# Performance work log

Measured on AMD Instinct MI355X. Metric: run time of the kernel, lower is better.

## Reference

```python
import jax, jax.numpy as jnp
import numpy as np

N = 50000      # nodes
E = 800000     # edges per relation (avg degree 16)
D = 128        # in_feat == out_feat
H = 4          # num_heads
DH = D // H    # head dim = 32
NEG_SLOPE = 0.2  # DGL GATConv default


def setup_inputs() -> dict:
    key = jax.random.key(0)
    ks = jax.random.split(key, 12)
    inp = {
        "x": jax.random.normal(ks[0], (N, D), jnp.float32),
        "W_r0": jax.random.normal(ks[1], (D, D), jnp.float32) * (1.0 / np.sqrt(D)),
        "attn_l_r0": jax.random.normal(ks[2], (H, DH), jnp.float32),
        "attn_r_r0": jax.random.normal(ks[3], (H, DH), jnp.float32),
        "W_r1": jax.random.normal(ks[4], (D, D), jnp.float32) * (1.0 / np.sqrt(D)),
        "attn_l_r1": jax.random.normal(ks[5], (H, DH), jnp.float32),
        "attn_r_r1": jax.random.normal(ks[6], (H, DH), jnp.float32),
        "loop_weight": jax.random.normal(ks[7], (D, D), jnp.float32) * (1.0 / np.sqrt(D)),
        "h_bias": jnp.zeros((D,), jnp.float32),
        "src_r0": jax.random.randint(ks[8], (E,), 0, N, jnp.int32),
        "dst_r0": jax.random.randint(ks[9], (E,), 0, N, jnp.int32),
        "src_r1": jax.random.randint(ks[10], (E,), 0, N, jnp.int32),
        "dst_r1": jax.random.randint(ks[11], (E,), 0, N, jnp.int32),
    }
    return inp


def _gat_conv(x, W, attn_l, attn_r, src, dst):
    """One DGL-style GATConv (no bias, no conv activation). Returns [N,H,DH]."""
    feat = (x @ W).reshape(N, H, DH)                 # projected features
    el = jnp.einsum('nhd,hd->nh', feat, attn_l)      # [N,H] attn on source
    er = jnp.einsum('nhd,hd->nh', feat, attn_r)      # [N,H] attn on dest
    e = jax.nn.leaky_relu(el[src] + er[dst], NEG_SLOPE)  # [E,H]
    # edge softmax over incoming edges of each dst node (stable)
    emax = jax.ops.segment_max(e, dst, num_segments=N)   # [N,H]
    ex = jnp.exp(e - emax[dst])                          # [E,H]
    denom = jax.ops.segment_sum(ex, dst, num_segments=N) # [N,H]
    alpha = ex / denom[dst]                              # [E,H]
    msg = feat[src] * alpha[:, :, None]                  # [E,H,DH]
    return jax.ops.segment_sum(msg, dst, num_segments=N) # [N,H,DH]


def reference(x, W_r0, attn_l_r0, attn_r_r0, W_r1, attn_l_r1, attn_r_r1,
              loop_weight, h_bias, src_r0, dst_r0, src_r1, dst_r1):
    # HeteroGraphConv with default 'sum' cross-relation aggregation
    h = _gat_conv(x, W_r0, attn_l_r0, attn_r_r0, src_r0, dst_r0) \
      + _gat_conv(x, W_r1, attn_l_r1, attn_r_r1, src_r1, dst_r1)
    h = h.reshape(N, H * DH)          # flatten heads -> [N, out_feat]
    h = h + x @ loop_weight           # self loop
    h = h + h_bias                    # bias
    h = jax.nn.relu(h)                # activation (dropout=0, no norm, no FFN)
    return h
```

## Files before the change

kernel.cpp:

```cpp
#include <hip/hip_runtime.h>
#include <hip/hip_bf16.h>

#define NN 50000
#define EE 800000
#define DD 128
#define HH 4
#define NEG_SLOPE 0.2f

#define BSH 9
#define NBUCK 98
#define CH 8192
#define NBLK 98
#define NSEG (2 * NBUCK * NBLK)
#define BKB (2 * NBLK)
#define SORTB (2 * NBUCK)
#define ELRB 3125
#define PJB ((NN + 127) / 128)
#define WB 192

typedef __attribute__((ext_vector_type(8))) short bf16x8;
typedef __attribute__((ext_vector_type(4))) float f32x4;
typedef __attribute__((ext_vector_type(8))) unsigned short ushrt8;

static __device__ __forceinline__ float bf2f(ushort u) {
    union { unsigned int ui; float f; } v; v.ui = ((unsigned int)u) << 16; return v.f;
}
static __device__ __forceinline__ void split1(float v, ushort& h, ushort& l) {
    __hip_bfloat16 hb = __float2bfloat16(v);
    float hf = __bfloat162float(hb);
    __hip_bfloat16 lb = __float2bfloat16(v - hf);
    h = *(ushort*)&hb; l = *(ushort*)&lb;
}

__global__ __launch_bounds__(256) void prep_kernel(
    const float* __restrict__ W0, const float* __restrict__ W1,
    const float* __restrict__ Wl,
    const float* __restrict__ al0, const float* __restrict__ ar0,
    const float* __restrict__ al1, const float* __restrict__ ar1,
    const int* __restrict__ dst0, const int* __restrict__ dst1,
    ushort* __restrict__ wt, float* __restrict__ uvec, int* __restrict__ hist)
{
    const int b = blockIdx.x;
    const int t = threadIdx.x;
    if (b < WB) {
        int idx = b * 256 + t;
        int m = idx >> 14, e = idx & 16383;
        const float* W = (m == 0) ? W0 : (m == 1) ? W1 : Wl;
        int k = e >> 7, n = e & 127;
        ushort h, l; split1(W[e], h, l);
        int q = m * 4 + (k >> 5);
        int kin8 = (k >> 3) & 3, ke = k & 7;
        int sw = n & 7;
        size_t base = (size_t)q * 8192 + n * 64;
        wt[base + (((0 | kin8) ^ sw) << 3) + ke] = h;
        wt[base + (((4 | kin8) ^ sw) << 3) + ke] = l;
    } else if (b < WB + BKB) {
        __shared__ int cnt[NBUCK];
        int hb = b - WB;
        int rel = hb >= NBLK;
        int ci = hb - rel * NBLK;
        const int* __restrict__ dstA = rel ? dst1 : dst0;
        if (t < NBUCK) cnt[t] = 0;
        __syncthreads();
        int lo = ci * CH, hi = min(lo + CH, EE);
        for (int i = lo + t; i < hi; i += 256)
            atomicAdd(&cnt[dstA[i] >> BSH], 1);
        __syncthreads();
        if (t < NBUCK)
            hist[((rel * NBUCK) + t) * NBLK + ci] = cnt[t];
    } else {
        #pragma unroll
        for (int j = 0; j < 8; ++j) {
            int idx = t * 8 + j;
            int v = idx >> 7, k = idx & 127;
            int rel = v >> 3, lr = (v >> 2) & 1, h = v & 3;
            const float* W = rel ? W1 : W0;
            const float* a = rel ? (lr ? ar1 : al1) : (lr ? ar0 : al0);
            float s = 0.f;
            for (int d2 = 0; d2 < 32; ++d2)
                s += W[k * 128 + h * 32 + d2] * a[h * 32 + d2];
            uvec[v * 128 + k] = s;
        }
    }
}

__global__ __launch_bounds__(256) void scan_kernel(
    const int* __restrict__ hist, int* __restrict__ base)
{
    __shared__ int wq[4];
    const int t = threadIdx.x;
    const int lane = t & 63, wv = t >> 6;
    const int st = t * 76;
    const int en = min(st + 76, NSEG);
    int sum = 0;
    for (int i = st; i < en; ++i) sum += hist[i];
    int incl = sum;
    #pragma unroll
    for (int off = 1; off < 64; off <<= 1) {
        int u = __shfl_up(incl, off);
        if (lane >= off) incl += u;
    }
    if (lane == 63) wq[wv] = incl;
    __syncthreads();
    int woff = 0;
    #pragma unroll
    for (int w = 0; w < 4; ++w) woff += (w < wv) ? wq[w] : 0;
    int run = woff + incl - sum;
    for (int i = st; i < en; ++i) { base[i] = run; run += hist[i]; }
}

__global__ __launch_bounds__(256) void bucketelr_kernel(
    const int* __restrict__ src0, const int* __restrict__ dst0,
    const int* __restrict__ src1, const int* __restrict__ dst1,
    const int* __restrict__ base, unsigned int* __restrict__ pk,
    const float* __restrict__ x, const float* __restrict__ uvec,
    float* __restrict__ el0, float* __restrict__ er0,
    float* __restrict__ el1, float* __restrict__ er1)
{
    __shared__ float sm[2048];
    const int t = threadIdx.x;

    if (blockIdx.x < BKB) {
        int* cnt = (int*)sm;
        int* bs  = cnt + 128;
        const int hb = blockIdx.x;
        const int rel = hb >= NBLK;
        const int ci = hb - rel * NBLK;
        const int* __restrict__ srcA = rel ? src1 : src0;
        const int* __restrict__ dstA = rel ? dst1 : dst0;
        if (t < NBUCK) {
            cnt[t] = 0;
            bs[t] = base[((rel * NBUCK) + t) * NBLK + ci];
        }
        __syncthreads();
        int lo = ci * CH, hi = min(lo + CH, EE);
        for (int i = lo + t; i < hi; i += 256) {
            int dd = dstA[i], ss = srcA[i];
            int bk = dd >> BSH;
            int rk = atomicAdd(&cnt[bk], 1);
            pk[bs[bk] + rk] = (unsigned int)ss | ((unsigned int)(dd & 511) << 17);
        }
        return;
    }

    for (int i = t; i < 2048; i += 256) sm[i] = uvec[i];
    __syncthreads();
    const int lane = t & 63, wave = t >> 6;
    const int l16 = lane & 15;
    const int r = (blockIdx.x - BKB) * 16 + wave * 4 + (lane >> 4);
    float xr[8];
    if (r < NN) {
        float4 a = *(const float4*)&x[(size_t)r * DD + l16 * 8];
        float4 b2 = *(const float4*)&x[(size_t)r * DD + l16 * 8 + 4];
        xr[0] = a.x; xr[1] = a.y; xr[2] = a.z; xr[3] = a.w;
        xr[4] = b2.x; xr[5] = b2.y; xr[6] = b2.z; xr[7] = b2.w;
    } else {
        #pragma unroll
        for (int j = 0; j < 8; ++j) xr[j] = 0.f;
    }
    float s[16];
    #pragma unroll
    for (int v = 0; v < 16; ++v) {
        float acc = 0.f;
        const float* u = &sm[v * 128 + l16 * 8];
        #pragma unroll
        for (int j = 0; j < 8; ++j) acc += xr[j] * u[j];
        s[v] = acc;
    }
    #pragma unroll
    for (int m = 1; m < 16; m <<= 1)
        #pragma unroll
        for (int v = 0; v < 16; ++v) s[v] += __shfl_xor(s[v], m);
    if (r < NN) {
        float val = s[0];
        #pragma unroll
        for (int v = 1; v < 16; ++v) val = (l16 == v) ? s[v] : val;
        float* p = (l16 & 8) ? ((l16 & 4) ? er1 : el1)
                             : ((l16 & 4) ? er0 : el0);
        p[(size_t)r * 4 + (l16 & 3)] = val;
    }
}

__global__ __launch_bounds__(256) void proj_kernel(
    const float* __restrict__ x, const ushort* __restrict__ wt,
    const float* __restrict__ bias,
    ushort* __restrict__ fb0, ushort* __restrict__ fb1,
    float* __restrict__ out)
{
    __shared__ ushort lds[2][8192];
    const int t = threadIdx.x;
    const int lane = t & 63, wave = t >> 6;
    const int l15 = lane & 15, lg = lane >> 4;
    const int rb = blockIdx.x * 128 + wave * 32;

    int ra0 = rb + l15;      if (ra0 > NN - 1) ra0 = NN - 1;
    int ra1 = rb + 16 + l15; if (ra1 > NN - 1) ra1 = NN - 1;
    const int kb = lg * 8;

    bf16x8 Ah0[4], Av0[4], Ah1[4], Av1[4];
    #pragma unroll
    for (int kc = 0; kc < 4; ++kc) {
        const float* p0 = &x[(size_t)ra0 * DD + kc * 32 + kb];
        const float* p1 = &x[(size_t)ra1 * DD + kc * 32 + kb];
        float4 f0a = *(const float4*)p0, f0b = *(const float4*)(p0 + 4);
        float4 f1a = *(const float4*)p1, f1b = *(const float4*)(p1 + 4);
        float t0[8] = {f0a.x, f0a.y, f0a.z, f0a.w, f0b.x, f0b.y, f0b.z, f0b.w};
        float t1[8] = {f1a.x, f1a.y, f1a.z, f1a.w, f1b.x, f1b.y, f1b.z, f1b.w};
        union { bf16x8 v; ushort u[8]; } H0, L0, H1, L1;
        #pragma unroll
        for (int j = 0; j < 8; ++j) {
            split1(t0[j], H0.u[j], L0.u[j]);
            split1(t1[j], H1.u[j], L1.u[j]);
        }
        Ah0[kc] = H0.v; Av0[kc] = L0.v;
        Ah1[kc] = H1.v; Av1[kc] = L1.v;
    }

    {
        const bf16x8* g = (const bf16x8*)wt;
        bf16x8* L = (bf16x8*)lds[0];
        #pragma unroll
        for (int i = 0; i < 4; ++i) L[t + i * 256] = g[t + i * 256];
    }

    for (int m = 0; m < 3; ++m) {
        f32x4 acc0[8], acc1[8];
        #pragma unroll
        for (int nt = 0; nt < 8; ++nt) {
            acc0[nt] = (f32x4){0.f, 0.f, 0.f, 0.f};
            acc1[nt] = (f32x4){0.f, 0.f, 0.f, 0.f};
        }

        #pragma unroll
        for (int kc = 0; kc < 4; ++kc) {
            const int q = m * 4 + kc;
            __syncthreads();
            bf16x8 st0, st1, st2, st3;
            const bool hasNext = (q < 11);
            if (hasNext) {
                const bf16x8* g = (const bf16x8*)(wt + (size_t)(q + 1) * 8192);
                st0 = g[t]; st1 = g[t + 256]; st2 = g[t + 512]; st3 = g[t + 768];
            }
            const ushort* __restrict__ L = lds[kc & 1];
            #pragma unroll
            for (int nt = 0; nt < 8; ++nt) {
                const int n = nt * 16 + l15;
                const int sw = n & 7;
                bf16x8 bh = *(const bf16x8*)&L[n * 64 + (((0 | lg) ^ sw) << 3)];
                bf16x8 bv = *(const bf16x8*)&L[n * 64 + (((4 | lg) ^ sw) << 3)];
                acc0[nt] = __builtin_amdgcn_mfma_f32_16x16x32_bf16(Ah0[kc], bh, acc0[nt], 0, 0, 0);
                acc0[nt] = __builtin_amdgcn_mfma_f32_16x16x32_bf16(Ah0[kc], bv, acc0[nt], 0, 0, 0);
                acc0[nt] = __builtin_amdgcn_mfma_f32_16x16x32_bf16(Av0[kc], bh, acc0[nt], 0, 0, 0);
                acc1[nt] = __builtin_amdgcn_mfma_f32_16x16x32_bf16(Ah1[kc], bh, acc1[nt], 0, 0, 0);
                acc1[nt] = __builtin_amdgcn_mfma_f32_16x16x32_bf16(Ah1[kc], bv, acc1[nt], 0, 0, 0);
                acc1[nt] = __builtin_amdgcn_mfma_f32_16x16x32_bf16(Av1[kc], bh, acc1[nt], 0, 0, 0);
            }
            if (hasNext) {
                bf16x8* Lw = (bf16x8*)lds[(kc & 1) ^ 1];
                Lw[t] = st0; Lw[t + 256] = st1; Lw[t + 512] = st2; Lw[t + 768] = st3;
            }
        }

        if (m < 2) {
            ushort* __restrict__ fb = m ? fb1 : fb0;
            #pragma unroll
            for (int tt = 0; tt < 2; ++tt)
                #pragma unroll
                for (int nt = 0; nt < 8; ++nt) {
                    const int col = nt * 16 + l15;
                    #pragma unroll
                    for (int r = 0; r < 4; ++r) {
                        const int row = rb + tt * 16 + lg * 4 + r;
                        const float v = tt ? acc1[nt][r] : acc0[nt][r];
                        if (row < NN) {
                            __hip_bfloat16 hb = __float2bfloat16(v);
                            fb[(size_t)row * DD + col] = *(ushort*)&hb;
                        }
                    }
                }
        } else {
            #pragma unroll
            for (int tt = 0; tt < 2; ++tt)
                #pragma unroll
                for (int nt = 0; nt < 8; ++nt) {
                    const int col = nt * 16 + l15;
                    const float bv = bias[col];
                    #pragma unroll
                    for (int r = 0; r < 4; ++r) {
                        const int row = rb + tt * 16 + lg * 4 + r;
                        const float v = tt ? acc1[nt][r] : acc0[nt][r];
                        if (row < NN) out[(size_t)row * DD + col] = v + bv;
                    }
                }
        }
    }
}

__global__ __launch_bounds__(256) void sort_kernel(
    const unsigned int* __restrict__ pk, const int* __restrict__ base,
    int* __restrict__ row0, int* __restrict__ row1, int* __restrict__ list)
{
    __shared__ int cnt[512];
    __shared__ int offs[512];
    __shared__ int wq[4];
    const int hb = blockIdx.x;
    const int t = threadIdx.x;
    const int lane = t & 63, wv = t >> 6;
    const int rel = hb >= NBUCK;
    const int bk = hb - rel * NBUCK;

    const int fs = base[((rel * NBUCK) + bk) * NBLK];
    const int fe = (rel == 1 && bk == NBUCK - 1) ? 2 * EE
                 : base[((rel * NBUCK) + bk + 1) * NBLK];

    cnt[t] = 0; cnt[t + 256] = 0;
    __syncthreads();
    for (int i = fs + t; i < fe; i += 256)
        atomicAdd(&cnt[pk[i] >> 17], 1);
    __syncthreads();

    int a = cnt[2 * t], bvl = cnt[2 * t + 1];
    int ps = a + bvl;
    int incl = ps;
    #pragma unroll
    for (int off = 1; off < 64; off <<= 1) {
        int u = __shfl_up(incl, off);
        if (lane >= off) incl += u;
    }
    if (lane == 63) wq[wv] = incl;
    __syncthreads();
    int woff = 0;
    #pragma unroll
    for (int w = 0; w < 4; ++w) woff += (w < wv) ? wq[w] : 0;
    int excl = woff + incl - ps;
    offs[2 * t] = excl;
    offs[2 * t + 1] = excl + a;
    __syncthreads();

    int* __restrict__ row = rel ? row1 : row0;
    const int fsLocal = fs - (rel ? EE : 0);
    const int d0 = bk << BSH;
    for (int j = t; j < 512; j += 256) {
        int d = d0 + j;
        if (d < NN) row[d] = fsLocal + offs[j] + cnt[j];
    }
    __syncthreads();

    for (int i = fs + t; i < fe; i += 256) {
        unsigned int u = pk[i];
        int ld = u >> 17;
        int p = atomicAdd(&offs[ld], 1);
        list[fs + p] = (int)(u & 0x1FFFF);
    }
}

__global__ __launch_bounds__(256) void agg_kernel(
    const int* __restrict__ row0, const int* __restrict__ list0,
    const float* __restrict__ el0, const float* __restrict__ er0,
    const int* __restrict__ row1, const int* __restrict__ list1,
    const float* __restrict__ el1, const float* __restrict__ er1,
    const ushort* __restrict__ fb0, const ushort* __restrict__ fb1,
    float* __restrict__ out)
{
    const int d = blockIdx.x * 4 + (threadIdx.x >> 6);
    const int lane = threadIdx.x & 63;
    if (d >= NN) return;
    const int g = lane >> 4;
    const int l16 = lane & 15;
    const int c = l16 * 8;
    const int h = l16 >> 2;

    float tot[8] = {0.f, 0.f, 0.f, 0.f, 0.f, 0.f, 0.f, 0.f};

    #pragma unroll
    for (int rel = 0; rel < 2; ++rel) {
        const int* __restrict__ rowA = rel ? row1 : row0;
        const int* __restrict__ lst  = rel ? list1 : list0;
        const float* __restrict__ elA = rel ? el1 : el0;
        const float* __restrict__ erA = rel ? er1 : er0;
        const ushort* __restrict__ fbA = rel ? fb1 : fb0;

        const int s0 = d ? rowA[d - 1] : 0, e0 = rowA[d];
        const float erh = erA[(size_t)d * 4 + h];
        float acc[8] = {0.f, 0.f, 0.f, 0.f, 0.f, 0.f, 0.f, 0.f};
        float den = 0.f;

        int i = s0 + g;
        float elvA = 0.f;
        ushrt8 fA = (ushrt8){0, 0, 0, 0, 0, 0, 0, 0};
        if (i < e0) {
            int s = lst[i];
            elvA = elA[(size_t)s * 4 + h];
            fA = *(const ushrt8*)&fbA[(size_t)s * DD + c];
        }
        while (i < e0) {
            const int inext = i + 4;
            float elvB = 0.f;
            ushrt8 fB = (ushrt8){0, 0, 0, 0, 0, 0, 0, 0};
            if (inext < e0) {
                int s = lst[inext];
                elvB = elA[(size_t)s * 4 + h];
                fB = *(const ushrt8*)&fbA[(size_t)s * DD + c];
            }
            float ev = elvA + erh;
            ev = ev > 0.f ? ev : NEG_SLOPE * ev;
            float w = __expf(ev);
            den += w;
            #pragma unroll
            for (int q = 0; q < 8; ++q) acc[q] += w * bf2f(fA[q]);
            i = inext; elvA = elvB; fA = fB;
        }

        den += __shfl_xor(den, 16); den += __shfl_xor(den, 32);
        #pragma unroll
        for (int q = 0; q < 8; ++q) {
            acc[q] += __shfl_xor(acc[q], 16);
            acc[q] += __shfl_xor(acc[q], 32);
        }
        if (e0 > s0) {
            float inv = 1.f / den;
            #pragma unroll
            for (int q = 0; q < 8; ++q) tot[q] += acc[q] * inv;
        }
    }

    if (g == 0) {
        float4 o1 = *(float4*)&out[(size_t)d * DD + c];
        float4 o2 = *(float4*)&out[(size_t)d * DD + c + 4];
        o1.x = fmaxf(o1.x + tot[0], 0.f); o1.y = fmaxf(o1.y + tot[1], 0.f);
        o1.z = fmaxf(o1.z + tot[2], 0.f); o1.w = fmaxf(o1.w + tot[3], 0.f);
        o2.x = fmaxf(o2.x + tot[4], 0.f); o2.y = fmaxf(o2.y + tot[5], 0.f);
        o2.z = fmaxf(o2.z + tot[6], 0.f); o2.w = fmaxf(o2.w + tot[7], 0.f);
        *(float4*)&out[(size_t)d * DD + c] = o1;
        *(float4*)&out[(size_t)d * DD + c + 4] = o2;
    }
}

extern "C" void kernel_launch(void* const* d_in, const int* in_sizes, int n_in,
                              void* d_out, int out_size, void* d_ws, size_t ws_size,
                              hipStream_t stream)
{
    const float* x    = (const float*)d_in[0];
    const float* W0   = (const float*)d_in[1];
    const float* al0  = (const float*)d_in[2];
    const float* ar0  = (const float*)d_in[3];
    const float* W1   = (const float*)d_in[4];
    const float* al1  = (const float*)d_in[5];
    const float* ar1  = (const float*)d_in[6];
    const float* Wl   = (const float*)d_in[7];
    const float* bias = (const float*)d_in[8];
    const int* src0   = (const int*)d_in[9];
    const int* dst0   = (const int*)d_in[10];
    const int* src1   = (const int*)d_in[11];
    const int* dst1   = (const int*)d_in[12];
    float* out = (float*)d_out;

    ushort* wsu = (ushort*)d_ws;
    ushort* fb0 = wsu;
    ushort* fb1 = fb0 + (size_t)NN * DD;
    ushort* wt  = fb1 + (size_t)NN * DD;
    float* uvec = (float*)(wt + 12 * 8192);
    float* el0  = uvec + 2048;
    float* er0  = el0 + (size_t)NN * HH;
    float* el1  = er0 + (size_t)NN * HH;
    float* er1  = el1 + (size_t)NN * HH;
    int* hist   = (int*)(er1 + (size_t)NN * HH);
    int* base   = hist + NSEG;
    int* row0   = base + NSEG;
    int* row1   = row0 + NN;
    unsigned int* pk = (unsigned int*)(row1 + NN);
    int* list   = (int*)(pk + (size_t)2 * EE);
    int* list0  = list;
    int* list1  = list + EE;

    prep_kernel<<<dim3(WB + BKB + 1), dim3(256), 0, stream>>>(
        W0, W1, Wl, al0, ar0, al1, ar1, dst0, dst1, wt, uvec, hist);

    scan_kernel<<<dim3(1), dim3(256), 0, stream>>>(hist, base);

    bucketelr_kernel<<<dim3(BKB + ELRB), dim3(256), 0, stream>>>(
        src0, dst0, src1, dst1, base, pk, x, uvec, el0, er0, el1, er1);

    proj_kernel<<<dim3(PJB), dim3(256), 0, stream>>>(
        x, wt, bias, fb0, fb1, out);

    sort_kernel<<<dim3(SORTB), dim3(256), 0, stream>>>(
        pk, base, row0, row1, list);

    agg_kernel<<<dim3((NN + 3) / 4), dim3(256), 0, stream>>>(
        row0, list0, el0, er0, row1, list1, el1, er1, fb0, fb1, out);
}
```

Before: 194.1 us.

## Pad per-destination edge lists to multiples of four with sentinel entries

The sort kernel now lays out each destination's neighbour list padded to a multiple of four, filling the slack with a sentinel value, and records a start offset plus count per node instead of CSR row ends. The aggregation kernel runs a fixed trip count with no per-iteration bounds checks and no manual software prefetch, masking sentinel edges by zeroing their weight. Offsets switch to 32-bit unsigned arithmetic. The aim is to remove divergent tail handling and branches from the gather loop, at the cost of extra padded reads and writes, an additional workspace region, and relying on the hardware to hide latency now that the explicit prefetch is gone.

```diff
diff --git a/kernel.cpp b/kernel.cpp
--- a/kernel.cpp
+++ b/kernel.cpp
@@ -17,6 +17,7 @@
 #define ELRB 3125
 #define PJB ((NN + 127) / 128)
 #define WB 192
+#define PADSLACK 1536
 
 typedef __attribute__((ext_vector_type(8))) short bf16x8;
 typedef __attribute__((ext_vector_type(4))) float f32x4;
@@ -298,10 +299,13 @@
 
 __global__ __launch_bounds__(256) void sort_kernel(
     const unsigned int* __restrict__ pk, const int* __restrict__ base,
-    int* __restrict__ row0, int* __restrict__ row1, int* __restrict__ list)
+    int* __restrict__ rowS0, int* __restrict__ rowS1,
+    int* __restrict__ cntD0, int* __restrict__ cntD1,
+    unsigned int* __restrict__ plist)
 {
     __shared__ int cnt[512];
-    __shared__ int offs[512];
+    __shared__ int offsP[512];
+    __shared__ int offsM[512];
     __shared__ int wq[4];
     const int hb = blockIdx.x;
     const int t = threadIdx.x;
@@ -312,6 +316,7 @@
     const int fs = base[((rel * NBUCK) + bk) * NBLK];
     const int fe = (rel == 1 && bk == NBUCK - 1) ? 2 * EE
                  : base[((rel * NBUCK) + bk + 1) * NBLK];
+    const int pbase = fs + hb * PADSLACK;
 
     cnt[t] = 0; cnt[t + 256] = 0;
     __syncthreads();
@@ -320,7 +325,8 @@
     __syncthreads();
 
     int a = cnt[2 * t], bvl = cnt[2 * t + 1];
-    int ps = a + bvl;
+    int aP = (a + 3) & ~3, bP = (bvl + 3) & ~3;
+    int ps = aP + bP;
     int incl = ps;
     #pragma unroll
     for (int off = 1; off < 64; off <<= 1) {
@@ -333,32 +339,38 @@
     #pragma unroll
     for (int w = 0; w < 4; ++w) woff += (w < wv) ? wq[w] : 0;
     int excl = woff + incl - ps;
-    offs[2 * t] = excl;
-    offs[2 * t + 1] = excl + a;
-    __syncthreads();
-
-    int* __restrict__ row = rel ? row1 : row0;
-    const int fsLocal = fs - (rel ? EE : 0);
+    offsP[2 * t] = excl;          offsM[2 * t] = excl;
+    offsP[2 * t + 1] = excl + aP; offsM[2 * t + 1] = excl + aP;
+    __syncthreads();
+
+    int* __restrict__ rowS = rel ? rowS1 : rowS0;
+    int* __restrict__ rcnt = rel ? cntD1 : cntD0;
     const int d0 = bk << BSH;
     for (int j = t; j < 512; j += 256) {
         int d = d0 + j;
-        if (d < NN) row[d] = fsLocal + offs[j] + cnt[j];
-    }
-    __syncthreads();
+        if (d < NN) { rowS[d] = pbase + offsP[j]; rcnt[d] = cnt[j]; }
+    }
 
     for (int i = fs + t; i < fe; i += 256) {
         unsigned int u = pk[i];
         int ld = u >> 17;
-        int p = atomicAdd(&offs[ld], 1);
-        list[fs + p] = (int)(u & 0x1FFFF);
+        int p = atomicAdd(&offsM[ld], 1);
+        plist[pbase + p] = u & 0x1FFFF;
+    }
+
+    for (int j = t; j < 512; j += 256) {
+        int st = offsP[j] + cnt[j];
+        int en = offsP[j] + ((cnt[j] + 3) & ~3);
+        for (int p = st; p < en; ++p) plist[pbase + p] = 0x80000000u;
     }
 }
 
 __global__ __launch_bounds__(256) void agg_kernel(
-    const int* __restrict__ row0, const int* __restrict__ list0,
+    const int* __restrict__ rowS0, const int* __restrict__ cntD0,
     const float* __restrict__ el0, const float* __restrict__ er0,
-    const int* __restrict__ row1, const int* __restrict__ list1,
+    const int* __restrict__ rowS1, const int* __restrict__ cntD1,
     const float* __restrict__ el1, const float* __restrict__ er1,
+    const unsigned int* __restrict__ plist,
     const ushort* __restrict__ fb0, const ushort* __restrict__ fb1,
     float* __restrict__ out)
 {
@@ -367,48 +379,38 @@
     if (d >= NN) return;
     const int g = lane >> 4;
     const int l16 = lane & 15;
-    const int c = l16 * 8;
+    const unsigned c = l16 * 8;
     const int h = l16 >> 2;
 
     float tot[8] = {0.f, 0.f, 0.f, 0.f, 0.f, 0.f, 0.f, 0.f};
 
     #pragma unroll
     for (int rel = 0; rel < 2; ++rel) {
-        const int* __restrict__ rowA = rel ? row1 : row0;
-        const int* __restrict__ lst  = rel ? list1 : list0;
+        const int* __restrict__ rowS = rel ? rowS1 : rowS0;
+        const int* __restrict__ rcnt = rel ? cntD1 : cntD0;
         const float* __restrict__ elA = rel ? el1 : el0;
         const float* __restrict__ erA = rel ? er1 : er0;
         const ushort* __restrict__ fbA = rel ? fb1 : fb0;
 
-        const int s0 = d ? rowA[d - 1] : 0, e0 = rowA[d];
-        const float erh = erA[(size_t)d * 4 + h];
+        const int s0 = rowS[d];
+        const int cn = rcnt[d];
+        const float erh = erA[(unsigned)(d * 4 + h)];
+        const int trips = (cn + 3) >> 2;
         float acc[8] = {0.f, 0.f, 0.f, 0.f, 0.f, 0.f, 0.f, 0.f};
         float den = 0.f;
 
-        int i = s0 + g;
-        float elvA = 0.f;
-        ushrt8 fA = (ushrt8){0, 0, 0, 0, 0, 0, 0, 0};
-        if (i < e0) {
-            int s = lst[i];
-            elvA = elA[(size_t)s * 4 + h];
-            fA = *(const ushrt8*)&fbA[(size_t)s * DD + c];
-        }
-        while (i < e0) {
-            const int inext = i + 4;
-            float elvB = 0.f;
-            ushrt8 fB = (ushrt8){0, 0, 0, 0, 0, 0, 0, 0};
-            if (inext < e0) {
-                int s = lst[inext];
-                elvB = elA[(size_t)s * 4 + h];
-                fB = *(const ushrt8*)&fbA[(size_t)s * DD + c];
-            }
-            float ev = elvA + erh;
+        unsigned ib = (unsigned)(s0 + g);
+        for (int k = 0; k < trips; ++k) {
+            unsigned u = plist[ib + 4u * k];
+            unsigned s = u & 0x1FFFFu;
+            float ev = elA[s * 4u + h] + erh;
             ev = ev > 0.f ? ev : NEG_SLOPE * ev;
             float w = __expf(ev);
+            w = (int)u < 0 ? 0.f : w;
             den += w;
+            ushrt8 f = *(const ushrt8*)&fbA[s * (unsigned)DD + c];
             #pragma unroll
-            for (int q = 0; q < 8; ++q) acc[q] += w * bf2f(fA[q]);
-            i = inext; elvA = elvB; fA = fB;
+            for (int q = 0; q < 8; ++q) acc[q] += w * bf2f(f[q]);
         }
 
         den += __shfl_xor(den, 16); den += __shfl_xor(den, 32);
@@ -417,7 +419,7 @@
             acc[q] += __shfl_xor(acc[q], 16);
             acc[q] += __shfl_xor(acc[q], 32);
         }
-        if (e0 > s0) {
+        if (cn > 0) {
             float inv = 1.f / den;
             #pragma unroll
             for (int q = 0; q < 8; ++q) tot[q] += acc[q] * inv;
@@ -466,12 +468,12 @@
     float* er1  = el1 + (size_t)NN * HH;
     int* hist   = (int*)(er1 + (size_t)NN * HH);
     int* base   = hist + NSEG;
-    int* row0   = base + NSEG;
-    int* row1   = row0 + NN;
-    unsigned int* pk = (unsigned int*)(row1 + NN);
-    int* list   = (int*)(pk + (size_t)2 * EE);
-    int* list0  = list;
-    int* list1  = list + EE;
+    int* rowS0  = base + NSEG;
+    int* rowS1  = rowS0 + NN;
+    int* cntD0  = rowS1 + NN;
+    int* cntD1  = cntD0 + NN;
+    unsigned int* pk    = (unsigned int*)(cntD1 + NN);
+    unsigned int* plist = pk + (size_t)2 * EE;
 
     prep_kernel<<<dim3(WB + BKB + 1), dim3(256), 0, stream>>>(
         W0, W1, Wl, al0, ar0, al1, ar1, dst0, dst1, wt, uvec, hist);
@@ -485,8 +487,8 @@
         x, wt, bias, fb0, fb1, out);
 
     sort_kernel<<<dim3(SORTB), dim3(256), 0, stream>>>(
-        pk, base, row0, row1, list);
+        pk, base, rowS0, rowS1, cntD0, cntD1, plist);
 
     agg_kernel<<<dim3((NN + 3) / 4), dim3(256), 0, stream>>>(
-        row0, list0, el0, er0, row1, list1, el1, er1, fb0, fb1, out);
-}
+        rowS0, cntD0, el0, er0, rowS1, cntD1, el1, er1, plist, fb0, fb1, out);
+}
```

Result: no change. 198.0 us (+2.0%).
